# Optimization experiments

Hardware: AMD Instinct MI355X
Metric: run time of the kernel (lower is better)

The kernel has to match this reference:

```python
import jax, jax.numpy as jnp
import numpy as np

CODEBOOK_SIZE = 8192
CODEBOOK_DIM = 1024
HIDDEN_DIM = 4096
OUT_DIM = 1024
B, M = 32, 576


def setup_inputs() -> dict:
    key = jax.random.key(0)
    k_idx, k_cb, k_w1, k_w2 = jax.random.split(key, 4)
    index = jax.random.randint(k_idx, (B, M), 0, CODEBOOK_SIZE, dtype=jnp.int32)
    # codebook initialized as sqrt(d) * randn, as in the torch module
    codebook = (CODEBOOK_DIM ** 0.5) * jax.random.normal(k_cb, (CODEBOOK_SIZE, CODEBOOK_DIM), dtype=jnp.float32)
    s1 = 1.0 / np.sqrt(CODEBOOK_DIM)
    s2 = 1.0 / np.sqrt(HIDDEN_DIM)
    W1 = s1 * jax.random.normal(k_w1, (CODEBOOK_DIM, HIDDEN_DIM), dtype=jnp.float32)
    b1 = jnp.zeros((HIDDEN_DIM,), dtype=jnp.float32)
    W2 = s2 * jax.random.normal(k_w2, (HIDDEN_DIM, OUT_DIM), dtype=jnp.float32)
    b2 = jnp.zeros((OUT_DIM,), dtype=jnp.float32)
    return {"index": index, "codebook": codebook, "W1": W1, "b1": b1, "W2": W2, "b2": b2}


def reference(index, codebook, W1, b1, W2, b2):
    # one_hot(index) @ codebook is mathematically an index gather:
    # quantized[b, m, :] = codebook[index[b, m], :]
    quantized = jnp.take(codebook, index, axis=0)  # [B, M, D]
    # Decoder_ff: 2-layer GELU MLP (D -> 4D -> D)
    h = jax.nn.gelu(jnp.einsum('bmd,dh->bmh', quantized, W1) + b1)
    rec = jnp.einsum('bmh,ho->bmo', h, W2) + b2
    return rec
```

## Files before the change

kernel.cpp:

```cpp
#include <hip/hip_runtime.h>
#include <stdint.h>

typedef __attribute__((ext_vector_type(8))) short s16x8;
typedef __attribute__((ext_vector_type(4))) float f32x4;

__device__ __forceinline__ short f2bf(float x) {
  uint32_t u = __builtin_bit_cast(uint32_t, x);
  u += 0x7FFFu + ((u >> 16) & 1u);
  return (short)(u >> 16);
}

__device__ __forceinline__ void gload16(void* l, const void* g) {
  __builtin_amdgcn_global_load_lds(
      (const __attribute__((address_space(1))) void*)g,
      (__attribute__((address_space(3))) void*)l, 16, 0, 0);
}

__device__ __forceinline__ float gelu_tanh(float x) {
  float u = 0.7978845608028654f * (x + 0.044715f * x * x * x);
  float e = __expf(2.0f * u);
  return x - x / (e + 1.0f);
}

__global__ void gather_cvt(const float* __restrict__ cb, const int* __restrict__ idx,
                           short* __restrict__ out) {
  int m = blockIdx.x * 2 + (threadIdx.x >> 7);
  int c = (threadIdx.x & 127) * 8;
  const float* s = cb + (size_t)idx[m] * 1024 + c;
  s16x8 o;
#pragma unroll
  for (int j = 0; j < 8; ++j) o[j] = f2bf(s[j]);
  *(s16x8*)(out + (size_t)m * 1024 + c) = o;
}

__global__ void cvt_T(const float* __restrict__ in, short* __restrict__ out, int K, int N) {
  int Kb = K >> 3;
  int t = blockIdx.x * 256 + threadIdx.x;
  if (t >= N * Kb) return;
  int n = t / Kb;
  int k8 = (t - n * Kb) * 8;
  const float* s = in + (size_t)k8 * N + n;
  s16x8 o;
#pragma unroll
  for (int j = 0; j < 8; ++j) o[j] = f2bf(s[(size_t)j * N]);
  *(s16x8*)(out + (size_t)n * K + k8) = o;
}

template <int MODE, int K, int N>
__global__ __launch_bounds__(512, 2) void gemmq(
    const short* __restrict__ A, const short* __restrict__ Bt,
    const float* __restrict__ bias, void* __restrict__ Cv) {
  constexpr int BM = 192, BN = 256;
  constexpr int AHS = BM * 64;
  constexpr int BHS = BN * 64;
  constexpr int BB = 2 * AHS;
  __shared__ short lds[2 * AHS + 3 * BHS];

  constexpr int NBN = N / BN;
  const int nwg = gridDim.x;
  int swz = blockIdx.x;
  swz = (swz & 7) * (nwg >> 3) + (swz >> 3);
  const int bm = swz / NBN, bn = swz - (swz / NBN) * NBN;

  const int tid = threadIdx.x;
  const int wid = tid >> 6, lane = tid & 63;
  const int wr = wid >> 2, wc = wid & 3;
  const int lr = lane & 15, hi = lane >> 4;

  const int sl = (tid & 7) ^ ((tid >> 3) & 7);
  const long rstep = (long)64 * K;
  const short* aptr = A + (long)(bm * BM + (tid >> 3)) * K + sl * 8;
  const short* bptr = Bt + (long)(bn * BN + (tid >> 3)) * K + sl * 8;
  const int wlds = wid * 512;

  const int aRB = (wr * 96 + lr) * 64;
  const int bRB = (wc * 64 + lr) * 64;
  const int sk0 = (hi ^ (lr & 7)) * 8;
  const int sk1 = ((4 + hi) ^ (lr & 7)) * 8;

  f32x4 acc[6][4] = {};
  s16x8 af[3][2], bf0[2][2], bf1[2][2];

  constexpr int NT = K >> 6;

#pragma unroll
  for (int r = 0; r < 3; ++r) gload16(&lds[r * 4096 + wlds], aptr + r * rstep);
#pragma unroll
  for (int r = 0; r < 4; ++r) gload16(&lds[BB + r * 4096 + wlds], bptr + r * rstep);
#pragma unroll
  for (int r = 0; r < 4; ++r) gload16(&lds[BB + BHS + r * 4096 + wlds], bptr + r * rstep + 64);
  asm volatile("s_waitcnt vmcnt(4)" ::: "memory");
  __builtin_amdgcn_s_barrier();

  int rb0 = BB, rb1 = BB + BHS, rb2 = BB + 2 * BHS;

  for (int t = 0; t < NT; ++t) {
    const int ca = (t & 1) * AHS;
    const int na = AHS - ca;
    const int ka = ((t + 1 < NT) ? (t + 1) : t) << 6;
    const int kb = ((t + 2 < NT) ? (t + 2) : t) << 6;

#pragma unroll
    for (int mi = 0; mi < 3; ++mi) {
      af[mi][0] = *(const s16x8*)&lds[ca + aRB + mi * 1024 + sk0];
      af[mi][1] = *(const s16x8*)&lds[ca + aRB + mi * 1024 + sk1];
    }
#pragma unroll
    for (int nj = 0; nj < 2; ++nj) {
      bf0[nj][0] = *(const s16x8*)&lds[rb0 + bRB + nj * 1024 + sk0];
      bf0[nj][1] = *(const s16x8*)&lds[rb0 + bRB + nj * 1024 + sk1];
    }
    gload16(&lds[na + 0 * 4096 + wlds], aptr + 0 * rstep + ka);
    gload16(&lds[na + 1 * 4096 + wlds], aptr + 1 * rstep + ka);
    __builtin_amdgcn_s_barrier();
    asm volatile("s_waitcnt lgkmcnt(0)" ::: "memory");
    __builtin_amdgcn_s_setprio(1);
#pragma unroll
    for (int mi = 0; mi < 3; ++mi)
#pragma unroll
      for (int nj = 0; nj < 2; ++nj)
#pragma unroll
        for (int ks = 0; ks < 2; ++ks)
          acc[mi][nj] = __builtin_amdgcn_mfma_f32_16x16x32_bf16(af[mi][ks], bf0[nj][ks], acc[mi][nj], 0, 0, 0);
    __builtin_amdgcn_s_setprio(0);
    __builtin_amdgcn_s_barrier();

#pragma unroll
    for (int nj = 0; nj < 2; ++nj) {
      bf1[nj][0] = *(const s16x8*)&lds[rb0 + bRB + (2 + nj) * 1024 + sk0];
      bf1[nj][1] = *(const s16x8*)&lds[rb0 + bRB + (2 + nj) * 1024 + sk1];
    }
    gload16(&lds[na + 2 * 4096 + wlds], aptr + 2 * rstep + ka);
    gload16(&lds[rb2 + 0 * 4096 + wlds], bptr + 0 * rstep + kb);
    __builtin_amdgcn_s_barrier();
    asm volatile("s_waitcnt lgkmcnt(0)" ::: "memory");
    __builtin_amdgcn_s_setprio(1);
#pragma unroll
    for (int mi = 0; mi < 3; ++mi)
#pragma unroll
      for (int nj = 0; nj < 2; ++nj)
#pragma unroll
        for (int ks = 0; ks < 2; ++ks)
          acc[mi][2 + nj] = __builtin_amdgcn_mfma_f32_16x16x32_bf16(af[mi][ks], bf1[nj][ks], acc[mi][2 + nj], 0, 0, 0);
    __builtin_amdgcn_s_setprio(0);
    __builtin_amdgcn_s_barrier();

#pragma unroll
    for (int mi = 0; mi < 3; ++mi) {
      af[mi][0] = *(const s16x8*)&lds[ca + aRB + (3 + mi) * 1024 + sk0];
      af[mi][1] = *(const s16x8*)&lds[ca + aRB + (3 + mi) * 1024 + sk1];
    }
    gload16(&lds[rb2 + 1 * 4096 + wlds], bptr + 1 * rstep + kb);
    gload16(&lds[rb2 + 2 * 4096 + wlds], bptr + 2 * rstep + kb);
    __builtin_amdgcn_s_barrier();
    asm volatile("s_waitcnt lgkmcnt(0)" ::: "memory");
    __builtin_amdgcn_s_setprio(1);
#pragma unroll
    for (int mi = 0; mi < 3; ++mi)
#pragma unroll
      for (int nj = 0; nj < 2; ++nj)
#pragma unroll
        for (int ks = 0; ks < 2; ++ks)
          acc[3 + mi][nj] = __builtin_amdgcn_mfma_f32_16x16x32_bf16(af[mi][ks], bf0[nj][ks], acc[3 + mi][nj], 0, 0, 0);
    __builtin_amdgcn_s_setprio(0);
    __builtin_amdgcn_s_barrier();

    gload16(&lds[rb2 + 3 * 4096 + wlds], bptr + 3 * rstep + kb);
    __builtin_amdgcn_s_setprio(1);
#pragma unroll
    for (int mi = 0; mi < 3; ++mi)
#pragma unroll
      for (int nj = 0; nj < 2; ++nj)
#pragma unroll
        for (int ks = 0; ks < 2; ++ks)
          acc[3 + mi][2 + nj] = __builtin_amdgcn_mfma_f32_16x16x32_bf16(af[mi][ks], bf1[nj][ks], acc[3 + mi][2 + nj], 0, 0, 0);
    __builtin_amdgcn_s_setprio(0);
    asm volatile("s_waitcnt vmcnt(4)" ::: "memory");
    __builtin_amdgcn_s_barrier();
    const int tmp = rb0; rb0 = rb1; rb1 = rb2; rb2 = tmp;
  }

  const int m0 = bm * BM + wr * 96 + hi * 4;
  const int n0 = bn * BN + wc * 64 + lr;
#pragma unroll
  for (int nj = 0; nj < 4; ++nj) {
    const int n = n0 + nj * 16;
    const float bv = bias[n];
#pragma unroll
    for (int mi = 0; mi < 6; ++mi) {
      f32x4 v = acc[mi][nj];
#pragma unroll
      for (int r = 0; r < 4; ++r) {
        const int m = m0 + mi * 16 + r;
        float x = v[r] + bv;
        if (MODE == 1) {
          ((short*)Cv)[(size_t)m * N + n] = f2bf(gelu_tanh(x));
        } else {
          ((float*)Cv)[(size_t)m * N + n] = x;
        }
      }
    }
  }
}

extern "C" void kernel_launch(void* const* d_in, const int* in_sizes, int n_in,
                              void* d_out, int out_size, void* d_ws, size_t ws_size,
                              hipStream_t stream) {
  const int* idx = (const int*)d_in[0];
  const float* cb = (const float*)d_in[1];
  const float* W1 = (const float*)d_in[2];
  const float* b1 = (const float*)d_in[3];
  const float* W2 = (const float*)d_in[4];
  const float* b2 = (const float*)d_in[5];
  float* out = (float*)d_out;

  const int Mtot = 32 * 576;

  char* ws = (char*)d_ws;
  short* aq = (short*)(ws);
  short* w1t = (short*)(ws + (size_t)40 * 1024 * 1024);
  short* w2t = (short*)(ws + (size_t)48 * 1024 * 1024);
  short* h = (short*)(ws + (size_t)56 * 1024 * 1024);

  gather_cvt<<<Mtot / 2, 256, 0, stream>>>(cb, idx, aq);
  cvt_T<<<2048, 256, 0, stream>>>(W1, w1t, 1024, 4096);
  cvt_T<<<2048, 256, 0, stream>>>(W2, w2t, 4096, 1024);

  size_t avail = (ws_size > (size_t)56 * 1024 * 1024) ? ws_size - (size_t)56 * 1024 * 1024 : 0;
  int nc = 1;
  while (nc < 8 && (size_t)(Mtot / nc) * 8192 > avail) nc <<= 1;
  const int Mc = Mtot / nc;

  for (int c = 0; c < nc; ++c) {
    gemmq<1, 1024, 4096><<<(Mc / 192) * 16, 512, 0, stream>>>(
        aq + (size_t)c * Mc * 1024, w1t, b1, (void*)h);
    gemmq<2, 4096, 1024><<<(Mc / 192) * 4, 512, 0, stream>>>(
        h, w2t, b2, (void*)(out + (size_t)c * Mc * 1024));
  }
}
```

Baseline: 446.4 us.

## Triple-buffer A tiles, double-buffer B, and remap workgroups per XCD

Swaps the LDS buffering roles so the A (M-side) tile gets three prefetch stages and the B tile two, with B loads issued one step ahead and A loads two steps ahead. It also drops the explicit lgkmcnt waits before the MFMA blocks. The workgroup-to-tile mapping is changed so each XCD gets a contiguous rectangular region of M×N tiles, which is meant to improve L2 reuse of both operands. The risks are a changed LDS footprint and relying on the compiler to insert the LDS read waits that were removed. The new mapping also assumes the grid divides evenly into eight XCDs times half of the N tiles.

Result: faster. 435.3 us (-2.5%).

```diff
diff --git a/kernel.cpp b/kernel.cpp
--- a/kernel.cpp
+++ b/kernel.cpp
@@ -47,20 +47,24 @@
 }
 
 template <int MODE, int K, int N>
-__global__ __launch_bounds__(512, 2) void gemmq(
+__global__ __launch_bounds__(512, 2) void gemmf(
     const short* __restrict__ A, const short* __restrict__ Bt,
     const float* __restrict__ bias, void* __restrict__ Cv) {
   constexpr int BM = 192, BN = 256;
   constexpr int AHS = BM * 64;
   constexpr int BHS = BN * 64;
-  constexpr int BB = 2 * AHS;
-  __shared__ short lds[2 * AHS + 3 * BHS];
+  constexpr int BB = 3 * AHS;
+  __shared__ short lds[3 * AHS + 2 * BHS];
 
   constexpr int NBN = N / BN;
+  constexpr int RBN = NBN / 2;
   const int nwg = gridDim.x;
-  int swz = blockIdx.x;
-  swz = (swz & 7) * (nwg >> 3) + (swz >> 3);
-  const int bm = swz / NBN, bn = swz - (swz / NBN) * NBN;
+  const int xcd = blockIdx.x & 7;
+  const int c = blockIdx.x >> 3;
+  const int RBM = (nwg >> 3) / RBN;
+  const int lbm = c / RBN, lbn = c - (c / RBN) * RBN;
+  const int bm = (xcd >> 1) * RBM + lbm;
+  const int bn = (xcd & 1) * RBN + lbn;
 
   const int tid = threadIdx.x;
   const int wid = tid >> 6, lane = tid & 63;
@@ -84,36 +88,35 @@
   constexpr int NT = K >> 6;
 
 #pragma unroll
-  for (int r = 0; r < 3; ++r) gload16(&lds[r * 4096 + wlds], aptr + r * rstep);
-#pragma unroll
   for (int r = 0; r < 4; ++r) gload16(&lds[BB + r * 4096 + wlds], bptr + r * rstep);
 #pragma unroll
-  for (int r = 0; r < 4; ++r) gload16(&lds[BB + BHS + r * 4096 + wlds], bptr + r * rstep + 64);
-  asm volatile("s_waitcnt vmcnt(4)" ::: "memory");
+  for (int r = 0; r < 3; ++r) gload16(&lds[0 * AHS + r * 4096 + wlds], aptr + r * rstep);
+#pragma unroll
+  for (int r = 0; r < 3; ++r) gload16(&lds[1 * AHS + r * 4096 + wlds], aptr + r * rstep + 64);
+  asm volatile("s_waitcnt vmcnt(3)" ::: "memory");
   __builtin_amdgcn_s_barrier();
 
-  int rb0 = BB, rb1 = BB + BHS, rb2 = BB + 2 * BHS;
+  int ra0 = 0, ra1 = AHS, ra2 = 2 * AHS;
 
   for (int t = 0; t < NT; ++t) {
-    const int ca = (t & 1) * AHS;
-    const int na = AHS - ca;
-    const int ka = ((t + 1 < NT) ? (t + 1) : t) << 6;
-    const int kb = ((t + 2 < NT) ? (t + 2) : t) << 6;
+    const int cbB = BB + (t & 1) * BHS;
+    const int nbB = BB + ((t + 1) & 1) * BHS;
+    const int kb = ((t + 1 < NT) ? (t + 1) : t) << 6;
+    const int ka = ((t + 2 < NT) ? (t + 2) : t) << 6;
 
 #pragma unroll
     for (int mi = 0; mi < 3; ++mi) {
-      af[mi][0] = *(const s16x8*)&lds[ca + aRB + mi * 1024 + sk0];
-      af[mi][1] = *(const s16x8*)&lds[ca + aRB + mi * 1024 + sk1];
+      af[mi][0] = *(const s16x8*)&lds[ra0 + aRB + mi * 1024 + sk0];
+      af[mi][1] = *(const s16x8*)&lds[ra0 + aRB + mi * 1024 + sk1];
     }
 #pragma unroll
     for (int nj = 0; nj < 2; ++nj) {
-      bf0[nj][0] = *(const s16x8*)&lds[rb0 + bRB + nj * 1024 + sk0];
-      bf0[nj][1] = *(const s16x8*)&lds[rb0 + bRB + nj * 1024 + sk1];
-    }
-    gload16(&lds[na + 0 * 4096 + wlds], aptr + 0 * rstep + ka);
-    gload16(&lds[na + 1 * 4096 + wlds], aptr + 1 * rstep + ka);
-    __builtin_amdgcn_s_barrier();
-    asm volatile("s_waitcnt lgkmcnt(0)" ::: "memory");
+      bf0[nj][0] = *(const s16x8*)&lds[cbB + bRB + nj * 1024 + sk0];
+      bf0[nj][1] = *(const s16x8*)&lds[cbB + bRB + nj * 1024 + sk1];
+    }
+    gload16(&lds[nbB + 0 * 4096 + wlds], bptr + 0 * rstep + kb);
+    gload16(&lds[nbB + 1 * 4096 + wlds], bptr + 1 * rstep + kb);
+    __builtin_amdgcn_s_barrier();
     __builtin_amdgcn_s_setprio(1);
 #pragma unroll
     for (int mi = 0; mi < 3; ++mi)
@@ -127,13 +130,12 @@
 
 #pragma unroll
     for (int nj = 0; nj < 2; ++nj) {
-      bf1[nj][0] = *(const s16x8*)&lds[rb0 + bRB + (2 + nj) * 1024 + sk0];
-      bf1[nj][1] = *(const s16x8*)&lds[rb0 + bRB + (2 + nj) * 1024 + sk1];
-    }
-    gload16(&lds[na + 2 * 4096 + wlds], aptr + 2 * rstep + ka);
-    gload16(&lds[rb2 + 0 * 4096 + wlds], bptr + 0 * rstep + kb);
-    __builtin_amdgcn_s_barrier();
-    asm volatile("s_waitcnt lgkmcnt(0)" ::: "memory");
+      bf1[nj][0] = *(const s16x8*)&lds[cbB + bRB + (2 + nj) * 1024 + sk0];
+      bf1[nj][1] = *(const s16x8*)&lds[cbB + bRB + (2 + nj) * 1024 + sk1];
+    }
+    gload16(&lds[nbB + 2 * 4096 + wlds], bptr + 2 * rstep + kb);
+    gload16(&lds[nbB + 3 * 4096 + wlds], bptr + 3 * rstep + kb);
+    __builtin_amdgcn_s_barrier();
     __builtin_amdgcn_s_setprio(1);
 #pragma unroll
     for (int mi = 0; mi < 3; ++mi)
@@ -147,13 +149,12 @@
 
 #pragma unroll
     for (int mi = 0; mi < 3; ++mi) {
-      af[mi][0] = *(const s16x8*)&lds[ca + aRB + (3 + mi) * 1024 + sk0];
-      af[mi][1] = *(const s16x8*)&lds[ca + aRB + (3 + mi) * 1024 + sk1];
-    }
-    gload16(&lds[rb2 + 1 * 4096 + wlds], bptr + 1 * rstep + kb);
-    gload16(&lds[rb2 + 2 * 4096 + wlds], bptr + 2 * rstep + kb);
-    __builtin_amdgcn_s_barrier();
-    asm volatile("s_waitcnt lgkmcnt(0)" ::: "memory");
+      af[mi][0] = *(const s16x8*)&lds[ra0 + aRB + (3 + mi) * 1024 + sk0];
+      af[mi][1] = *(const s16x8*)&lds[ra0 + aRB + (3 + mi) * 1024 + sk1];
+    }
+    gload16(&lds[ra2 + 0 * 4096 + wlds], aptr + 0 * rstep + ka);
+    gload16(&lds[ra2 + 1 * 4096 + wlds], aptr + 1 * rstep + ka);
+    __builtin_amdgcn_s_barrier();
     __builtin_amdgcn_s_setprio(1);
 #pragma unroll
     for (int mi = 0; mi < 3; ++mi)
@@ -165,7 +166,7 @@
     __builtin_amdgcn_s_setprio(0);
     __builtin_amdgcn_s_barrier();
 
-    gload16(&lds[rb2 + 3 * 4096 + wlds], bptr + 3 * rstep + kb);
+    gload16(&lds[ra2 + 2 * 4096 + wlds], aptr + 2 * rstep + ka);
     __builtin_amdgcn_s_setprio(1);
 #pragma unroll
     for (int mi = 0; mi < 3; ++mi)
@@ -175,9 +176,9 @@
         for (int ks = 0; ks < 2; ++ks)
           acc[3 + mi][2 + nj] = __builtin_amdgcn_mfma_f32_16x16x32_bf16(af[mi][ks], bf1[nj][ks], acc[3 + mi][2 + nj], 0, 0, 0);
     __builtin_amdgcn_s_setprio(0);
-    asm volatile("s_waitcnt vmcnt(4)" ::: "memory");
-    __builtin_amdgcn_s_barrier();
-    const int tmp = rb0; rb0 = rb1; rb1 = rb2; rb2 = tmp;
+    asm volatile("s_waitcnt vmcnt(3)" ::: "memory");
+    __builtin_amdgcn_s_barrier();
+    const int tmp = ra0; ra0 = ra1; ra1 = ra2; ra2 = tmp;
   }
 
   const int m0 = bm * BM + wr * 96 + hi * 4;
@@ -232,9 +233,9 @@
   const int Mc = Mtot / nc;
 
   for (int c = 0; c < nc; ++c) {
-    gemmq<1, 1024, 4096><<<(Mc / 192) * 16, 512, 0, stream>>>(
+    gemmf<1, 1024, 4096><<<(Mc / 192) * 16, 512, 0, stream>>>(
         aq + (size_t)c * Mc * 1024, w1t, b1, (void*)h);
-    gemmq<2, 4096, 1024><<<(Mc / 192) * 4, 512, 0, stream>>>(
+    gemmf<2, 4096, 1024><<<(Mc / 192) * 4, 512, 0, stream>>>(
         h, w2t, b2, (void*)(out + (size_t)c * Mc * 1024));
   }
 }
```
